# Kernel tuning notes

Hardware: AMD Instinct MI355X
Metric: run time of the kernel (lower is better)

## Reference

```python
import jax, jax.numpy as jnp
import numpy as np
import math

BS, SEQ, EMB, BD = 4, 2048, 512, 8
H = EMB // BD


def setup_inputs() -> dict:
    key = jax.random.key(0)
    ks = jax.random.split(key, 7)
    s = lambda fan: 1.0 / np.sqrt(fan)
    x = jax.random.normal(ks[0], (BS, SEQ, EMB), jnp.float32)
    # gen_block: Linear(EMB, EMB*BD) -> ReLU -> Linear(EMB*BD, EMB*BD)
    W1 = jax.random.normal(ks[1], (EMB * BD, EMB), jnp.float32) * s(EMB)
    b1 = jnp.zeros((EMB * BD,), jnp.float32)
    W2 = jax.random.normal(ks[2], (EMB * BD, EMB * BD), jnp.float32) * s(EMB * BD)
    b2 = jnp.zeros((EMB * BD,), jnp.float32)
    # gen_value: Linear(EMB, EMB) -> ReLU -> Linear(EMB, EMB)
    V1 = jax.random.normal(ks[3], (EMB, EMB), jnp.float32) * s(EMB)
    c1 = jnp.zeros((EMB,), jnp.float32)
    V2 = jax.random.normal(ks[4], (EMB, EMB), jnp.float32) * s(EMB)
    c2 = jnp.zeros((EMB,), jnp.float32)
    a0 = jax.random.normal(ks[5], (1, H, BD), jnp.float32)
    return {"x": x, "W1": W1, "b1": b1, "W2": W2, "b2": b2,
            "V1": V1, "c1": c1, "V2": V2, "c2": c2, "a0": a0}


def _forward(x, W1, b1, W2, b2, V1, c1, V2, c2, a0):
    bs, seq_len, emb = x.shape
    bd = BD
    h = emb // bd
    # block transition matrices: [bs, seq, h, bd, bd]
    blk = jax.nn.relu(x @ W1.T + b1) @ W2.T + b2
    blk = blk.reshape(bs, seq_len, h, bd, bd)
    blk = blk - blk.mean(axis=-2, keepdims=True)
    # p=1.2 norm over rows (dim=-2), then max over columns (dim=-1)
    norm = jnp.sum(jnp.abs(blk) ** 1.2, axis=-2, keepdims=True) ** (1.0 / 1.2)
    blk = blk / jnp.max(norm, axis=-1, keepdims=True)
    # values: [bs, seq, h, bd]
    v = (jax.nn.relu(x @ V1.T + c1) @ V2.T + c2).reshape(bs, seq_len, h, bd)

    log2_L = int(math.ceil(math.log2(seq_len + 1)))
    L = 2 ** log2_L
    n_zero = L - seq_len - 1
    # prepend a0 as initial state, pad to length L
    ev = jnp.concatenate([jnp.broadcast_to(a0, (bs, h, bd))[:, None], v], axis=1)
    a = jnp.pad(ev, ((0, 0), (0, n_zero), (0, 0), (0, 0)))  # [bs, L, h, bd]
    As = jnp.pad(blk, ((0, 0), (0, n_zero), (0, 0), (0, 0), (0, 0)))[:, :, None]  # [bs, L-1, 1, h, bd, bd]

    # Blelloch-style tree scan; log2_L levels, shapes shrink along n and grow along c
    for _ in range(log2_L):
        c = As.shape[2] * 2
        a = a.reshape(bs, L // c, c, h, bd)
        a1, a2 = a[:, :, :c // 2], a[:, :, c // 2:]
        coef = As[:, ::2]          # [bs, L//c, c//2, h, bd, bd]
        remain = As[:, 1::2]       # [bs, L//c - 1, c//2, h, bd, bd]
        prodd = jnp.einsum('bnchij,bnhjk->bnchik', coef[:, 1:], remain[:, :, -1])
        remain = jnp.concatenate([remain, prodd], axis=2)
        a2 = a2 + jnp.einsum('bnchij,bnhj->bnchi', coef, a1[:, :, -1])
        a = jnp.concatenate([a1, a2], axis=2)
        As = remain

    return a.reshape(bs, L, emb)[:, 1:seq_len + 1]


def reference(x, W1, b1, W2, b2, V1, c1, V2, c2, a0):
    return _forward(x, W1, b1, W2, b2, V1, c1, V2, c2, a0)
```

## Files before the change

### kernel.cpp

```cpp
#include <hip/hip_runtime.h>
#include <hip/hip_bf16.h>
#include <cstddef>


typedef _Float16 f16;
typedef _Float16 f16x4 __attribute__((ext_vector_type(4)));
typedef _Float16 f16x8 __attribute__((ext_vector_type(8)));
typedef float f32x4 __attribute__((ext_vector_type(4)));

#define LDP 40

__global__ __launch_bounds__(256)
void split_kernel(const float* __restrict__ in, f16* __restrict__ hi,
                  f16* __restrict__ lo, int n) {
  const int idx = (blockIdx.x * 256 + threadIdx.x) * 4;
  if (idx >= n) return;
  float4 v = *(const float4*)(in + idx);
  f16x4 h, l;
  h.x = (f16)v.x; l.x = (f16)(v.x - (float)h.x);
  h.y = (f16)v.y; l.y = (f16)(v.y - (float)h.y);
  h.z = (f16)v.z; l.z = (f16)(v.z - (float)h.z);
  h.w = (f16)v.w; l.w = (f16)(v.w - (float)h.w);
  *(f16x4*)(hi + idx) = h;
  *(f16x4*)(lo + idx) = l;
}

__device__ inline void stage_f32(const float* __restrict__ src, int ldk, int k0,
                                 f16* shi, f16* slo, int tid) {
  const int row = tid >> 1, kb = (tid & 1) << 4;
  const float* p = src + (size_t)row * ldk + k0 + kb;
#pragma unroll
  for (int q = 0; q < 4; ++q) {
    float4 v = *(const float4*)(p + q * 4);
    f16x4 h, l;
    h.x = (f16)v.x; l.x = (f16)(v.x - (float)h.x);
    h.y = (f16)v.y; l.y = (f16)(v.y - (float)h.y);
    h.z = (f16)v.z; l.z = (f16)(v.z - (float)h.z);
    h.w = (f16)v.w; l.w = (f16)(v.w - (float)h.w);
    *(f16x4*)&shi[row * LDP + kb + q * 4] = h;
    *(f16x4*)&slo[row * LDP + kb + q * 4] = l;
  }
}

__device__ inline void stage_pk(const unsigned int* __restrict__ src, int ldk, int k0,
                                f16* shi, f16* slo, int tid) {
  const int row = tid >> 1, kb = (tid & 1) << 4;
  const unsigned int* p = src + (size_t)row * ldk + k0 + kb;
#pragma unroll
  for (int q = 0; q < 4; ++q) {
    uint4 v = *(const uint4*)(p + q * 4);
    ushort4 hu, lu;
    hu.x = (unsigned short)(v.x & 0xffff); lu.x = (unsigned short)(v.x >> 16);
    hu.y = (unsigned short)(v.y & 0xffff); lu.y = (unsigned short)(v.y >> 16);
    hu.z = (unsigned short)(v.z & 0xffff); lu.z = (unsigned short)(v.z >> 16);
    hu.w = (unsigned short)(v.w & 0xffff); lu.w = (unsigned short)(v.w >> 16);
    *(ushort4*)&shi[row * LDP + kb + q * 4] = hu;
    *(ushort4*)&slo[row * LDP + kb + q * 4] = lu;
  }
}

template<int AFMT, int MODE>
__global__ __launch_bounds__(256)
void gemm_mfma(const void* __restrict__ Av, const float* __restrict__ B,
               const float* __restrict__ bias, void* __restrict__ Ov,
               int M, int N, int K, int roff) {
  __shared__ f16 sAhi[128 * LDP];
  __shared__ f16 sAlo[128 * LDP];
  __shared__ f16 sBhi[128 * LDP];
  __shared__ f16 sBlo[128 * LDP];
  const int tid = threadIdx.x;
  const int m0 = blockIdx.y << 7, n0 = blockIdx.x << 7;
  const int lane = tid & 63, wid = tid >> 6;
  const int wr = wid >> 1, wc = wid & 1;

  f32x4 acc[4][4];
#pragma unroll
  for (int m = 0; m < 4; ++m)
#pragma unroll
    for (int n = 0; n < 4; ++n) acc[m][n] = (f32x4)0.f;

  const int fr = lane & 15, fk = (lane >> 4) << 3;

  for (int k0 = 0; k0 < K; k0 += 32) {
    __syncthreads();
    if (AFMT == 0)
      stage_f32((const float*)Av + (size_t)m0 * K, K, k0, sAhi, sAlo, tid);
    else
      stage_pk((const unsigned int*)Av + (size_t)m0 * K, K, k0, sAhi, sAlo, tid);
    stage_f32(B + (size_t)n0 * K, K, k0, sBhi, sBlo, tid);
    __syncthreads();

    f16x8 ah[4], al[4], bh[4], bl[4];
#pragma unroll
    for (int m = 0; m < 4; ++m) {
      const int r = wr * 64 + m * 16 + fr;
      ah[m] = *(const f16x8*)&sAhi[r * LDP + fk];
      al[m] = *(const f16x8*)&sAlo[r * LDP + fk];
    }
#pragma unroll
    for (int n = 0; n < 4; ++n) {
      const int r = wc * 64 + n * 16 + fr;
      bh[n] = *(const f16x8*)&sBhi[r * LDP + fk];
      bl[n] = *(const f16x8*)&sBlo[r * LDP + fk];
    }
#pragma unroll
    for (int m = 0; m < 4; ++m)
#pragma unroll
      for (int n = 0; n < 4; ++n) {
        acc[m][n] = __builtin_amdgcn_mfma_f32_16x16x32_f16(ah[m], bh[n], acc[m][n], 0, 0, 0);
        acc[m][n] = __builtin_amdgcn_mfma_f32_16x16x32_f16(ah[m], bl[n], acc[m][n], 0, 0, 0);
        acc[m][n] = __builtin_amdgcn_mfma_f32_16x16x32_f16(al[m], bh[n], acc[m][n], 0, 0, 0);
      }
  }

  const int fq = lane >> 4;
  float bz[4];
#pragma unroll
  for (int n = 0; n < 4; ++n) bz[n] = bias[n0 + wc * 64 + n * 16 + fr];

#pragma unroll
  for (int m = 0; m < 4; ++m)
#pragma unroll
    for (int n = 0; n < 4; ++n) {
      const int col = n0 + wc * 64 + n * 16 + fr;
#pragma unroll
      for (int r = 0; r < 4; ++r) {
        const int row = m0 + wr * 64 + m * 16 + fq * 4 + r;
        float v = acc[m][n][r] + bz[n];
        if (MODE == 0 || MODE == 4) {
          v = fmaxf(v, 0.f);
          f16 h = (f16)v;
          f16 l = (f16)(v - (float)h);
          if (MODE == 0) {
            unsigned pk = ((unsigned)__builtin_bit_cast(unsigned short, l) << 16)
                        | (unsigned)__builtin_bit_cast(unsigned short, h);
            ((unsigned*)Ov)[(size_t)row * N + col] = pk;
          } else {
            f16* Hhi = (f16*)Ov;
            f16* Hlo = Hhi + (size_t)M * N;
            Hhi[(size_t)row * N + col] = h;
            Hlo[(size_t)row * N + col] = l;
          }
        } else {
          const int grow = roff + row;
          const int bb = grow >> 11, s = grow & 2047;
          if (MODE == 2) {
            ((float*)Ov)[(((size_t)(bb * 64 + (col >> 6)) * 2048 + s) << 6) + (col & 63)] = v;
          } else {
            ((float*)Ov)[(((size_t)(bb * 64 + (col >> 3)) * 2048 + s) << 3) + (col & 7)] = v;
          }
        }
      }
    }
}

__global__ __launch_bounds__(256)
void gemm2_dma(const f16* __restrict__ Ahi, const f16* __restrict__ Alo,
               const f16* __restrict__ Bhi, const f16* __restrict__ Blo,
               const float* __restrict__ bias, float* __restrict__ O,
               int M, int N, int K, int roff) {
  __shared__ f16 sA[2][128 * 64];
  __shared__ f16 sB[2][128 * 64];
  const int tid = threadIdx.x, lane = tid & 63, wid = tid >> 6;
  const int m0 = blockIdx.y << 7, n0 = blockIdx.x << 7;
  const int wr = wid >> 1, wc = wid & 1;
  const int fr = lane & 15, g = lane >> 4;

  f32x4 acc[4][4];
#pragma unroll
  for (int m = 0; m < 4; ++m)
#pragma unroll
    for (int n = 0; n < 4; ++n) acc[m][n] = (f32x4)0.f;

  const f16* gsrc = (wid == 0) ? Ahi + (size_t)m0 * K
                  : (wid == 1) ? Alo + (size_t)m0 * K
                  : (wid == 2) ? Bhi + (size_t)n0 * K
                               : Blo + (size_t)n0 * K;
  f16* ldst = (wid == 0) ? sA[0] : (wid == 1) ? sA[1]
            : (wid == 2) ? sB[0] : sB[1];
  const int lrow = lane >> 3;
  const int lc = lane & 7;

  for (int k0 = 0; k0 < K; k0 += 64) {
    __syncthreads();
#pragma unroll
    for (int i = 0; i < 16; ++i) {
      const int r = i * 8 + lrow;
      const int sg = (lc - r) & 7;
      const f16* sp = gsrc + (size_t)r * K + k0 + sg * 8;
      __builtin_amdgcn_global_load_lds(
          (const __attribute__((address_space(1))) unsigned int*)sp,
          (__attribute__((address_space(3))) unsigned int*)(ldst + i * 512),
          16, 0, 0);
    }
    __syncthreads();

#pragma unroll
    for (int kk = 0; kk < 2; ++kk) {
      f16x8 ah[4], al[4], bh[4], bl[4];
#pragma unroll
      for (int m = 0; m < 4; ++m) {
        const int r = wr * 64 + m * 16 + fr;
        const int off = r * 64 + ((((kk << 2) + g) + r) & 7) * 8;
        ah[m] = *(const f16x8*)&sA[0][off];
        al[m] = *(const f16x8*)&sA[1][off];
      }
#pragma unroll
      for (int n = 0; n < 4; ++n) {
        const int r = wc * 64 + n * 16 + fr;
        const int off = r * 64 + ((((kk << 2) + g) + r) & 7) * 8;
        bh[n] = *(const f16x8*)&sB[0][off];
        bl[n] = *(const f16x8*)&sB[1][off];
      }
#pragma unroll
      for (int m = 0; m < 4; ++m)
#pragma unroll
        for (int n = 0; n < 4; ++n) {
          acc[m][n] = __builtin_amdgcn_mfma_f32_16x16x32_f16(ah[m], bh[n], acc[m][n], 0, 0, 0);
          acc[m][n] = __builtin_amdgcn_mfma_f32_16x16x32_f16(ah[m], bl[n], acc[m][n], 0, 0, 0);
          acc[m][n] = __builtin_amdgcn_mfma_f32_16x16x32_f16(al[m], bh[n], acc[m][n], 0, 0, 0);
        }
    }
  }

  const int fq = lane >> 4;
  float bz[4];
#pragma unroll
  for (int n = 0; n < 4; ++n) bz[n] = bias[n0 + wc * 64 + n * 16 + fr];

#pragma unroll
  for (int m = 0; m < 4; ++m) {
#pragma unroll
    for (int r = 0; r < 4; ++r) {
      float v[4];
#pragma unroll
      for (int n = 0; n < 4; ++n) v[n] = acc[m][n][r] + bz[n];
      float s = v[0] + v[1] + v[2] + v[3];
      s += __shfl_xor(s, 8);
      const float mean = s * 0.125f;
      float t = 0.f;
#pragma unroll
      for (int n = 0; n < 4; ++n) {
        v[n] -= mean;
        t += exp2f(1.2f * log2f(fabsf(v[n])));
      }
      t += __shfl_xor(t, 8);
      float nrm = exp2f((1.0f / 1.2f) * log2f(t));
      nrm = fmaxf(nrm, __shfl_xor(nrm, 1));
      nrm = fmaxf(nrm, __shfl_xor(nrm, 2));
      nrm = fmaxf(nrm, __shfl_xor(nrm, 4));
      const float inv = 1.f / nrm;
      const int row = m0 + wr * 64 + m * 16 + fq * 4 + r;
      const int grow = roff + row;
      const int bb = grow >> 11, ss = grow & 2047;
#pragma unroll
      for (int n = 0; n < 4; ++n) {
        const int col = n0 + wc * 64 + n * 16 + fr;
        O[(((size_t)(bb * 64 + (col >> 6)) * 2048 + ss) << 6) + (col & 63)] = v[n] * inv;
      }
    }
  }
}

__global__ __launch_bounds__(256)
void norm_kernel(float* __restrict__ BLKT) {
  const int task = (blockIdx.x << 2) + (threadIdx.x >> 6);
  const int lane = threadIdx.x & 63;
  float* p = BLKT + (size_t)task * 64;
  float x = p[lane];
  float m = x;
  m += __shfl_xor(m, 8);
  m += __shfl_xor(m, 16);
  m += __shfl_xor(m, 32);
  x -= m * 0.125f;
  float ax = fabsf(x);
  float t = exp2f(1.2f * log2f(ax));
  t += __shfl_xor(t, 8);
  t += __shfl_xor(t, 16);
  t += __shfl_xor(t, 32);
  float nrm = exp2f((1.0f / 1.2f) * log2f(t));
  float mx = nrm;
  mx = fmaxf(mx, __shfl_xor(mx, 1));
  mx = fmaxf(mx, __shfl_xor(mx, 2));
  mx = fmaxf(mx, __shfl_xor(mx, 4));
  p[lane] = x / mx;
}

#define SCH2 16
#define SEGL 128
#define NSEG 16

__global__ __launch_bounds__(256)
void scan_part1(const float* __restrict__ BLKT, const float* __restrict__ VT,
                float* __restrict__ Msum, float* __restrict__ Csum) {
  __shared__ __align__(16) float Abuf[4][2][SCH2 * 64];
  __shared__ __align__(16) float vbuf[4][2][SCH2 * 8];
  const int w = threadIdx.x >> 6, lane = threadIdx.x & 63;
  const int id = blockIdx.x * 4 + w;
  const int stream = id >> 4, t = id & 15;
  const int i = lane >> 3, j = lane & 7;
  const float* Ab = BLKT + (size_t)stream * (2048 * 64) + (size_t)t * (SEGL * 64);
  const float* Vb = VT + (size_t)stream * (2048 * 8) + (size_t)t * (SEGL * 8);

  float m = (i == j) ? 1.f : 0.f;
  float cj = 0.f;

  float4 ra[4]; float2 rv;
  auto loadc = [&](int c) {
    const float* sA = Ab + c * (SCH2 * 64);
#pragma unroll
    for (int q = 0; q < 4; ++q) ra[q] = *(const float4*)(sA + q * 256 + lane * 4);
    rv = *(const float2*)(Vb + c * (SCH2 * 8) + lane * 2);
  };
  auto store_lds = [&](int slot) {
#pragma unroll
    for (int q = 0; q < 4; ++q)
      *(float4*)&Abuf[w][slot][q * 256 + lane * 4] = ra[q];
    *(float2*)&vbuf[w][slot][lane * 2] = rv;
  };

  loadc(0); store_lds(0);
  int cur = 0;
  const int NC = SEGL / SCH2;
  for (int c = 0; c < NC; ++c) {
    if (c + 1 < NC) loadc(c + 1);
#pragma unroll
    for (int s = 0; s < SCH2; ++s) {
      const float aij = Abuf[w][cur][s * 64 + lane];
      float p = aij * cj;
      p += __shfl_xor(p, 1);
      p += __shfl_xor(p, 2);
      p += __shfl_xor(p, 4);
      const float cn = p + vbuf[w][cur][s * 8 + i];
      cj = __shfl(cn, j << 3);
      float arow[8];
      *(float4*)&arow[0] = *(const float4*)&Abuf[w][cur][s * 64 + i * 8];
      *(float4*)&arow[4] = *(const float4*)&Abuf[w][cur][s * 64 + i * 8 + 4];
      float mn = 0.f;
#pragma unroll
      for (int k = 0; k < 8; ++k)
        mn = fmaf(arow[k], __shfl(m, (k << 3) | j), mn);
      m = mn;
    }
    if (c + 1 < NC) store_lds(cur ^ 1);
    cur ^= 1;
  }
  Msum[(size_t)id * 64 + lane] = m;
  if (lane < 8) Csum[(size_t)id * 8 + lane] = cj;
}

__global__ __launch_bounds__(64)
void scan_part2(const float* __restrict__ Msum, const float* __restrict__ Csum,
                const float* __restrict__ a0, float* __restrict__ Ybnd) {
  const int stream = blockIdx.x;
  const int lane = threadIdx.x;
  const int i = lane >> 3, j = lane & 7;
  const int h = stream & 63;
  float y = a0[h * 8 + j];
  for (int t = 0; t < NSEG; ++t) {
    const size_t sid = (size_t)stream * NSEG + t;
    if (lane < 8) Ybnd[sid * 8 + lane] = y;
    float p = Msum[sid * 64 + lane] * y;
    p += __shfl_xor(p, 1);
    p += __shfl_xor(p, 2);
    p += __shfl_xor(p, 4);
    const float yn = p + Csum[sid * 8 + i];
    y = __shfl(yn, j << 3);
  }
}

__global__ __launch_bounds__(256)
void scan_part3(const float* __restrict__ BLKT, const float* __restrict__ VT,
                const float* __restrict__ Ybnd, float* __restrict__ out) {
  __shared__ __align__(16) float Abuf[4][2][SCH2 * 64];
  __shared__ __align__(16) float vbuf[4][2][SCH2 * 8];
  const int w = threadIdx.x >> 6, lane = threadIdx.x & 63;
  const int id = blockIdx.x * 4 + w;
  const int stream = id >> 4, t = id & 15;
  const int b = stream >> 6, h = stream & 63;
  const int i = lane >> 3, j = lane & 7;
  const float* Ab = BLKT + (size_t)stream * (2048 * 64) + (size_t)t * (SEGL * 64);
  const float* Vb = VT + (size_t)stream * (2048 * 8) + (size_t)t * (SEGL * 8);
  float* ob = out + (size_t)b * (2048 * 512) + (size_t)(t * SEGL) * 512 + h * 8;

  float y = Ybnd[(size_t)id * 8 + j];

  float4 ra[4]; float2 rv;
  auto loadc = [&](int c) {
    const float* sA = Ab + c * (SCH2 * 64);
#pragma unroll
    for (int q = 0; q < 4; ++q) ra[q] = *(const float4*)(sA + q * 256 + lane * 4);
    rv = *(const float2*)(Vb + c * (SCH2 * 8) + lane * 2);
  };
  auto store_lds = [&](int slot) {
#pragma unroll
    for (int q = 0; q < 4; ++q)
      *(float4*)&Abuf[w][slot][q * 256 + lane * 4] = ra[q];
    *(float2*)&vbuf[w][slot][lane * 2] = rv;
  };

  loadc(0); store_lds(0);
  int cur = 0;
  const int NC = SEGL / SCH2;
  for (int c = 0; c < NC; ++c) {
    if (c + 1 < NC) loadc(c + 1);
#pragma unroll
    for (int s = 0; s < SCH2; ++s) {
      const float aij = Abuf[w][cur][s * 64 + lane];
      float p = aij * y;
      p += __shfl_xor(p, 1);
      p += __shfl_xor(p, 2);
      p += __shfl_xor(p, 4);
      const float yn = p + vbuf[w][cur][s * 8 + i];
      if (j == 0) ob[(size_t)(c * SCH2 + s) * 512 + i] = yn;
      y = __shfl(yn, j << 3);
    }
    if (c + 1 < NC) store_lds(cur ^ 1);
    cur ^= 1;
  }
}

extern "C" void kernel_launch(void* const* d_in, const int* in_sizes, int n_in,
                              void* d_out, int out_size, void* d_ws, size_t ws_size,
                              hipStream_t stream) {
  const float* x  = (const float*)d_in[0];
  const float* W1 = (const float*)d_in[1];
  const float* b1 = (const float*)d_in[2];
  const float* W2 = (const float*)d_in[3];
  const float* b2 = (const float*)d_in[4];
  const float* V1 = (const float*)d_in[5];
  const float* c1 = (const float*)d_in[6];
  const float* V2 = (const float*)d_in[7];
  const float* c2 = (const float*)d_in[8];
  const float* a0 = (const float*)d_in[9];
  float* out = (float*)d_out;

  dim3 blk(256);
  const size_t NEED_A = 252968960ull;

  if (ws_size >= NEED_A) {
    char* base = (char*)d_ws;
    float* BLKT   = (float*)base;
    float* VT     = (float*)(base + 134217728ull);
    f16*   W2hi   = (f16*)(base + 150994944ull);
    f16*   W2lo   = (f16*)(base + 184549376ull);
    f16*   H1hi   = (f16*)(base + 218103808ull);
    unsigned* HVs = (unsigned*)(base + 218103808ull);
    float* Msum   = (float*)(base + 251658240ull);
    float* Csum   = (float*)(base + 252706816ull);
    float* Ybnd   = (float*)(base + 252837888ull);

    split_kernel<<<16384, blk, 0, stream>>>(W2, W2hi, W2lo, 16777216);
    for (int c = 0; c < 4; ++c) {
      const float* xc = x + (size_t)c * 2048 * 512;
      gemm_mfma<0, 4><<<dim3(32, 16), blk, 0, stream>>>(xc, W1, b1, H1hi, 2048, 4096, 512, 0);
      gemm2_dma<<<dim3(32, 16), blk, 0, stream>>>(
          H1hi, H1hi + (size_t)2048 * 4096, W2hi, W2lo, b2, BLKT,
          2048, 4096, 4096, c * 2048);
    }
    gemm_mfma<0, 0><<<dim3(4, 64), blk, 0, stream>>>(x, V1, c1, HVs, 8192, 512, 512, 0);
    gemm_mfma<1, 3><<<dim3(4, 64), blk, 0, stream>>>(HVs, V2, c2, VT, 8192, 512, 512, 0);
    scan_part1<<<1024, blk, 0, stream>>>(BLKT, VT, Msum, Csum);
    scan_part2<<<256, 64, 0, stream>>>(Msum, Csum, a0, Ybnd);
    scan_part3<<<1024, blk, 0, stream>>>(BLKT, VT, Ybnd, out);
  } else {
    float* ws = (float*)d_ws;
    float* BLKT = ws;
    float* VT   = ws + 33554432ull;
    unsigned* H1s = (unsigned*)(ws + 37748736ull);
    unsigned* HVs = H1s;
    float* Msum = ws + 46137344ull;
    float* Csum = ws + 46399488ull;
    float* Ybnd = ws + 46432256ull;

    for (int c = 0; c < 4; ++c) {
      const float* xc = x + (size_t)c * 2048 * 512;
      gemm_mfma<0, 0><<<dim3(32, 16), blk, 0, stream>>>(xc, W1, b1, H1s, 2048, 4096, 512, 0);
      gemm_mfma<1, 2><<<dim3(32, 16), blk, 0, stream>>>(H1s, W2, b2, BLKT, 2048, 4096, 4096, c * 2048);
    }
    norm_kernel<<<131072, blk, 0, stream>>>(BLKT);
    gemm_mfma<0, 0><<<dim3(4, 64), blk, 0, stream>>>(x, V1, c1, HVs, 8192, 512, 512, 0);
    gemm_mfma<1, 3><<<dim3(4, 64), blk, 0, stream>>>(HVs, V2, c2, VT, 8192, 512, 512, 0);
    scan_part1<<<1024, blk, 0, stream>>>(BLKT, VT, Msum, Csum);
    scan_part2<<<256, 64, 0, stream>>>(Msum, Csum, a0, Ybnd);
    scan_part3<<<1024, blk, 0, stream>>>(BLKT, VT, Ybnd, out);
  }
}
```

Measured before the change: 1.040 ms.

## Route all GEMMs through pre-split f16 DMA-to-LDS kernel with three-term MFMA

Adds a templated gemm_dma2 kernel that stages pre-split hi/lo f16 operands straight into swizzled LDS with global_load_lds, double buffered, one wave per operand. Three-term f16 MFMA products emulate fp32 accuracy. W1, V1, V2 and each x chunk are now pre-split so the first-layer and value GEMMs also use the DMA path instead of converting fp32 in registers. The value-branch GEMMs move into the per-chunk loop. The change needs a larger workspace, and the old fallback path without norm fusion is removed.

```diff
diff --git a/kernel.cpp b/kernel.cpp
--- a/kernel.cpp
+++ b/kernel.cpp
@@ -23,6 +23,155 @@
   h.w = (f16)v.w; l.w = (f16)(v.w - (float)h.w);
   *(f16x4*)(hi + idx) = h;
   *(f16x4*)(lo + idx) = l;
+}
+
+template<int EPI>
+__global__ __launch_bounds__(256, 1)
+void gemm_dma2(const f16* __restrict__ Ahi, const f16* __restrict__ Alo,
+               const f16* __restrict__ Bhi, const f16* __restrict__ Blo,
+               const float* __restrict__ bias, void* __restrict__ Ov,
+               int M, int N, int K, int roff) {
+  __shared__ f16 S[2][4][128 * 64];
+  const int tid = threadIdx.x, lane = tid & 63, wid = tid >> 6;
+  const int m0 = blockIdx.y << 7, n0 = blockIdx.x << 7;
+  const int wr = wid >> 1, wc = wid & 1;
+  const int fr = lane & 15, g = lane >> 4;
+  const int lrow = lane >> 3, lc = lane & 7;
+  const int sg = (lc - lrow) & 7;
+
+  f32x4 acc[4][4];
+#pragma unroll
+  for (int m = 0; m < 4; ++m)
+#pragma unroll
+    for (int n = 0; n < 4; ++n) acc[m][n] = (f32x4)0.f;
+
+  const f16* gsrc = (wid == 0) ? Ahi + (size_t)m0 * K
+                  : (wid == 1) ? Alo + (size_t)m0 * K
+                  : (wid == 2) ? Bhi + (size_t)n0 * K
+                               : Blo + (size_t)n0 * K;
+
+  auto stage = [&](int b, int k0) {
+    f16* ld = &S[b][wid][0];
+#pragma unroll
+    for (int i = 0; i < 16; ++i) {
+      const int r = i * 8 + lrow;
+      const f16* sp = gsrc + (size_t)r * K + k0 + sg * 8;
+      __builtin_amdgcn_global_load_lds(
+          (const __attribute__((address_space(1))) unsigned int*)sp,
+          (__attribute__((address_space(3))) unsigned int*)(ld + i * 512),
+          16, 0, 0);
+    }
+  };
+
+  const int NT = K >> 6;
+  stage(0, 0);
+  __syncthreads();
+  int cur = 0;
+  for (int t = 0; t < NT; ++t) {
+    if (t + 1 < NT) stage(cur ^ 1, (t + 1) << 6);
+#pragma unroll
+    for (int kk = 0; kk < 2; ++kk) {
+      f16x8 ah[4], al[4], bh[4], bl[4];
+#pragma unroll
+      for (int m = 0; m < 4; ++m) {
+        const int r = wr * 64 + m * 16 + fr;
+        const int off = r * 64 + (((kk << 2) + g + r) & 7) * 8;
+        ah[m] = *(const f16x8*)&S[cur][0][off];
+        al[m] = *(const f16x8*)&S[cur][1][off];
+      }
+#pragma unroll
+      for (int n = 0; n < 4; ++n) {
+        const int r = wc * 64 + n * 16 + fr;
+        const int off = r * 64 + (((kk << 2) + g + r) & 7) * 8;
+        bh[n] = *(const f16x8*)&S[cur][2][off];
+        bl[n] = *(const f16x8*)&S[cur][3][off];
+      }
+#pragma unroll
+      for (int m = 0; m < 4; ++m)
+#pragma unroll
+        for (int n = 0; n < 4; ++n) {
+          acc[m][n] = __builtin_amdgcn_mfma_f32_16x16x32_f16(ah[m], bh[n], acc[m][n], 0, 0, 0);
+          acc[m][n] = __builtin_amdgcn_mfma_f32_16x16x32_f16(ah[m], bl[n], acc[m][n], 0, 0, 0);
+          acc[m][n] = __builtin_amdgcn_mfma_f32_16x16x32_f16(al[m], bh[n], acc[m][n], 0, 0, 0);
+        }
+    }
+    __syncthreads();
+    cur ^= 1;
+  }
+
+  const int fq = lane >> 4;
+  float bz[4];
+#pragma unroll
+  for (int n = 0; n < 4; ++n) bz[n] = bias[n0 + wc * 64 + n * 16 + fr];
+
+  if (EPI == 0) {
+    f16* Ohi = (f16*)Ov;
+    f16* Olo = Ohi + (size_t)M * N;
+#pragma unroll
+    for (int m = 0; m < 4; ++m)
+#pragma unroll
+      for (int n = 0; n < 4; ++n) {
+        const int col = n0 + wc * 64 + n * 16 + fr;
+#pragma unroll
+        for (int r = 0; r < 4; ++r) {
+          const int row = m0 + wr * 64 + m * 16 + fq * 4 + r;
+          float v = fmaxf(acc[m][n][r] + bz[n], 0.f);
+          f16 h = (f16)v;
+          f16 l = (f16)(v - (float)h);
+          Ohi[(size_t)row * N + col] = h;
+          Olo[(size_t)row * N + col] = l;
+        }
+      }
+  } else if (EPI == 1) {
+    float* O = (float*)Ov;
+#pragma unroll
+    for (int m = 0; m < 4; ++m) {
+#pragma unroll
+      for (int r = 0; r < 4; ++r) {
+        float v[4];
+#pragma unroll
+        for (int n = 0; n < 4; ++n) v[n] = acc[m][n][r] + bz[n];
+        float s = v[0] + v[1] + v[2] + v[3];
+        s += __shfl_xor(s, 8);
+        const float mean = s * 0.125f;
+        float t = 0.f;
+#pragma unroll
+        for (int n = 0; n < 4; ++n) {
+          v[n] -= mean;
+          t += exp2f(1.2f * log2f(fabsf(v[n])));
+        }
+        t += __shfl_xor(t, 8);
+        float nrm = exp2f((1.0f / 1.2f) * log2f(t));
+        nrm = fmaxf(nrm, __shfl_xor(nrm, 1));
+        nrm = fmaxf(nrm, __shfl_xor(nrm, 2));
+        nrm = fmaxf(nrm, __shfl_xor(nrm, 4));
+        const float inv = 1.f / nrm;
+        const int row = m0 + wr * 64 + m * 16 + fq * 4 + r;
+        const int grow = roff + row;
+        const int bb = grow >> 11, ss = grow & 2047;
+#pragma unroll
+        for (int n = 0; n < 4; ++n) {
+          const int col = n0 + wc * 64 + n * 16 + fr;
+          O[(((size_t)(bb * 64 + (col >> 6)) * 2048 + ss) << 6) + (col & 63)] = v[n] * inv;
+        }
+      }
+    }
+  } else {
+    float* O = (float*)Ov;
+#pragma unroll
+    for (int m = 0; m < 4; ++m)
+#pragma unroll
+      for (int n = 0; n < 4; ++n) {
+        const int col = n0 + wc * 64 + n * 16 + fr;
+#pragma unroll
+        for (int r = 0; r < 4; ++r) {
+          const int row = m0 + wr * 64 + m * 16 + fq * 4 + r;
+          const int grow = roff + row;
+          const int bb = grow >> 11, ss = grow & 2047;
+          O[(((size_t)(bb * 64 + (col >> 3)) * 2048 + ss) << 3) + (col & 7)] = acc[m][n][r] + bz[n];
+        }
+      }
+  }
 }
 
 __device__ inline void stage_f32(const float* __restrict__ src, int ldk, int k0,
@@ -262,30 +411,6 @@
   }
 }
 
-__global__ __launch_bounds__(256)
-void norm_kernel(float* __restrict__ BLKT) {
-  const int task = (blockIdx.x << 2) + (threadIdx.x >> 6);
-  const int lane = threadIdx.x & 63;
-  float* p = BLKT + (size_t)task * 64;
-  float x = p[lane];
-  float m = x;
-  m += __shfl_xor(m, 8);
-  m += __shfl_xor(m, 16);
-  m += __shfl_xor(m, 32);
-  x -= m * 0.125f;
-  float ax = fabsf(x);
-  float t = exp2f(1.2f * log2f(ax));
-  t += __shfl_xor(t, 8);
-  t += __shfl_xor(t, 16);
-  t += __shfl_xor(t, 32);
-  float nrm = exp2f((1.0f / 1.2f) * log2f(t));
-  float mx = nrm;
-  mx = fmaxf(mx, __shfl_xor(mx, 1));
-  mx = fmaxf(mx, __shfl_xor(mx, 2));
-  mx = fmaxf(mx, __shfl_xor(mx, 4));
-  p[lane] = x / mx;
-}
-
 #define SCH2 16
 #define SEGL 128
 #define NSEG 16
@@ -436,9 +561,52 @@
   float* out = (float*)d_out;
 
   dim3 blk(256);
-  const size_t NEED_A = 252968960ull;
-
-  if (ws_size >= NEED_A) {
+  const size_t NEED_NEW = 267649024ull;
+  const size_t NEED_A   = 252968960ull;
+
+  if (ws_size >= NEED_NEW) {
+    char* base = (char*)d_ws;
+    float* BLKT = (float*)base;
+    float* VT   = (float*)(base + 134217728ull);
+    f16* W2hi   = (f16*)(base + 150994944ull);
+    f16* W2lo   = (f16*)(base + 184549376ull);
+    f16* H1hi   = (f16*)(base + 218103808ull);
+    f16* xchi   = (f16*)(base + 251658240ull);
+    f16* xclo   = (f16*)(base + 253755392ull);
+    f16* W1hi   = (f16*)(base + 255852544ull);
+    f16* W1lo   = (f16*)(base + 260046848ull);
+    f16* V1hi   = (f16*)(base + 264241152ull);
+    f16* V1lo   = (f16*)(base + 264765440ull);
+    f16* V2hi   = (f16*)(base + 265289728ull);
+    f16* V2lo   = (f16*)(base + 265814016ull);
+    float* Msum = (float*)(base + 266338304ull);
+    float* Csum = (float*)(base + 267386880ull);
+    float* Ybnd = (float*)(base + 267517952ull);
+    f16* HVhi   = H1hi;
+
+    split_kernel<<<16384, blk, 0, stream>>>(W2, W2hi, W2lo, 16777216);
+    split_kernel<<<2048, blk, 0, stream>>>(W1, W1hi, W1lo, 2097152);
+    split_kernel<<<256, blk, 0, stream>>>(V1, V1hi, V1lo, 262144);
+    split_kernel<<<256, blk, 0, stream>>>(V2, V2hi, V2lo, 262144);
+
+    for (int c = 0; c < 4; ++c) {
+      const float* xc = x + (size_t)c * 2048 * 512;
+      split_kernel<<<1024, blk, 0, stream>>>(xc, xchi, xclo, 1048576);
+      gemm_dma2<0><<<dim3(32, 16), blk, 0, stream>>>(
+          xchi, xclo, W1hi, W1lo, b1, H1hi, 2048, 4096, 512, 0);
+      gemm_dma2<1><<<dim3(32, 16), blk, 0, stream>>>(
+          H1hi, H1hi + (size_t)2048 * 4096, W2hi, W2lo, b2, BLKT,
+          2048, 4096, 4096, c * 2048);
+      gemm_dma2<0><<<dim3(4, 16), blk, 0, stream>>>(
+          xchi, xclo, V1hi, V1lo, c1, HVhi, 2048, 512, 512, 0);
+      gemm_dma2<2><<<dim3(4, 16), blk, 0, stream>>>(
+          HVhi, HVhi + (size_t)2048 * 512, V2hi, V2lo, c2, VT,
+          2048, 512, 512, c * 2048);
+    }
+    scan_part1<<<1024, blk, 0, stream>>>(BLKT, VT, Msum, Csum);
+    scan_part2<<<256, 64, 0, stream>>>(Msum, Csum, a0, Ybnd);
+    scan_part3<<<1024, blk, 0, stream>>>(BLKT, VT, Ybnd, out);
+  } else {
     char* base = (char*)d_ws;
     float* BLKT   = (float*)base;
     float* VT     = (float*)(base + 134217728ull);
@@ -463,26 +631,5 @@
     scan_part1<<<1024, blk, 0, stream>>>(BLKT, VT, Msum, Csum);
     scan_part2<<<256, 64, 0, stream>>>(Msum, Csum, a0, Ybnd);
     scan_part3<<<1024, blk, 0, stream>>>(BLKT, VT, Ybnd, out);
-  } else {
-    float* ws = (float*)d_ws;
-    float* BLKT = ws;
-    float* VT   = ws + 33554432ull;
-    unsigned* H1s = (unsigned*)(ws + 37748736ull);
-    unsigned* HVs = H1s;
-    float* Msum = ws + 46137344ull;
-    float* Csum = ws + 46399488ull;
-    float* Ybnd = ws + 46432256ull;
-
-    for (int c = 0; c < 4; ++c) {
-      const float* xc = x + (size_t)c * 2048 * 512;
-      gemm_mfma<0, 0><<<dim3(32, 16), blk, 0, stream>>>(xc, W1, b1, H1s, 2048, 4096, 512, 0);
-      gemm_mfma<1, 2><<<dim3(32, 16), blk, 0, stream>>>(H1s, W2, b2, BLKT, 2048, 4096, 4096, c * 2048);
-    }
-    norm_kernel<<<131072, blk, 0, stream>>>(BLKT);
-    gemm_mfma<0, 0><<<dim3(4, 64), blk, 0, stream>>>(x, V1, c1, HVs, 8192, 512, 512, 0);
-    gemm_mfma<1, 3><<<dim3(4, 64), blk, 0, stream>>>(HVs, V2, c2, VT, 8192, 512, 512, 0);
-    scan_part1<<<1024, blk, 0, stream>>>(BLKT, VT, Msum, Csum);
-    scan_part2<<<256, 64, 0, stream>>>(Msum, Csum, a0, Ybnd);
-    scan_part3<<<1024, blk, 0, stream>>>(BLKT, VT, Ybnd, out);
-  }
-}
+  }
+}
```

Result: slower. 1.258 ms (+21.0%).
